# Optimization experiments

Hardware: AMD Instinct MI355X
Metric: run time of the kernel (lower is better)

Reference implementation:

```python
import jax, jax.numpy as jnp
import numpy as np

N = 50000
E = 800000
F_IN = 128
CONV_OUT = 128
CONV_LAYERS = 2
LSTM_OUT = 128
OUT_CH = 64


def setup_inputs() -> dict:
    key = jax.random.key(0)
    ks = jax.random.split(key, 16)
    s = 0.05
    inp = {
        "x": jax.random.normal(ks[0], (N, F_IN), jnp.float32),
        "edge_index": jax.random.randint(ks[1], (2, E), 0, N, dtype=jnp.int32),
        "edge_weight": jax.random.uniform(ks[2], (E,), jnp.float32),
        "H": jax.random.normal(ks[3], (1, N, LSTM_OUT), jnp.float32),
        "C": jax.random.normal(ks[4], (1, N, LSTM_OUT), jnp.float32),
        # GatedGraphConv params
        "ggc_weight": jax.random.normal(ks[5], (CONV_LAYERS, CONV_OUT, CONV_OUT), jnp.float32) * s,
        "gru_wih": jax.random.normal(ks[6], (3 * CONV_OUT, CONV_OUT), jnp.float32) * s,
        "gru_whh": jax.random.normal(ks[7], (3 * CONV_OUT, CONV_OUT), jnp.float32) * s,
        "gru_bih": jax.random.normal(ks[8], (3 * CONV_OUT,), jnp.float32) * s,
        "gru_bhh": jax.random.normal(ks[9], (3 * CONV_OUT,), jnp.float32) * s,
        # LSTM params (single layer, gate order i,f,g,o as in torch)
        "lstm_wih": jax.random.normal(ks[10], (4 * LSTM_OUT, CONV_OUT), jnp.float32) * s,
        "lstm_whh": jax.random.normal(ks[11], (4 * LSTM_OUT, LSTM_OUT), jnp.float32) * s,
        "lstm_bih": jax.random.normal(ks[12], (4 * LSTM_OUT,), jnp.float32) * s,
        "lstm_bhh": jax.random.normal(ks[13], (4 * LSTM_OUT,), jnp.float32) * s,
        # output linear
        "lin_w": jax.random.normal(ks[14], (OUT_CH, LSTM_OUT), jnp.float32) * s,
        "lin_b": jax.random.normal(ks[15], (OUT_CH,), jnp.float32) * s,
    }
    return inp


def reference(x, edge_index, edge_weight, H, C, ggc_weight, gru_wih, gru_whh,
              gru_bih, gru_bhh, lstm_wih, lstm_whh, lstm_bih, lstm_bhh, lin_w, lin_b):
    n = x.shape[0]
    out_dim = ggc_weight.shape[1]
    # GatedGraphConv: zero-pad input features up to out_dim if needed
    if x.shape[1] < out_dim:
        h = jnp.pad(x, ((0, 0), (0, out_dim - x.shape[1])))
    else:
        h = x
    src, dst = edge_index[0], edge_index[1]
    for i in range(ggc_weight.shape[0]):
        m = h @ ggc_weight[i]                      # [N, out]
        msg = m[src] * edge_weight[:, None]        # gather + weight, [E, out]
        agg = jax.ops.segment_sum(msg, dst, num_segments=n)  # scatter-add
        # GRUCell(input=agg, hidden=h)
        gi = agg @ gru_wih.T + gru_bih
        gh = h @ gru_whh.T + gru_bhh
        i_r, i_z, i_n = jnp.split(gi, 3, axis=-1)
        h_r, h_z, h_n = jnp.split(gh, 3, axis=-1)
        r = jax.nn.sigmoid(i_r + h_r)
        z = jax.nn.sigmoid(i_z + h_z)
        ncand = jnp.tanh(i_n + r * h_n)
        h = (1.0 - z) * ncand + z * h
    # single-timestep, single-layer LSTM (torch gate order i,f,g,o)
    hx, cx = H[0], C[0]
    gates = h @ lstm_wih.T + lstm_bih + hx @ lstm_whh.T + lstm_bhh
    ig, fg, gg, og = jnp.split(gates, 4, axis=-1)
    ig = jax.nn.sigmoid(ig)
    fg = jax.nn.sigmoid(fg)
    gg = jnp.tanh(gg)
    og = jax.nn.sigmoid(og)
    c_new = fg * cx + ig * gg
    h_new = og * jnp.tanh(c_new)
    out = jax.nn.relu(h_new) @ lin_w.T + lin_b     # relu then linear head
    return (out, h_new[None], c_new[None])
```

## Files before the change

### kernel.cpp

```cpp
#include <hip/hip_runtime.h>
#include <math.h>

#define N_NODES 50000
#define E_EDGES 800000
#define KD 128
#define NBLK_SCAN 196
#define RT_TILES 3125
#define CELL_RB 128
#define CELL_STRIDE (CELL_RB * 4)
#define CELL_BLOCKS 1024

typedef __attribute__((ext_vector_type(8))) short bf16x8;
typedef __attribute__((ext_vector_type(4))) float f32x4;

__device__ __forceinline__ float fsig(float x) { return 1.f / (1.f + __expf(-x)); }
__device__ __forceinline__ float ftanh(float x) { return 1.f - 2.f / (1.f + __expf(2.f * x)); }

__device__ __forceinline__ unsigned short f2bf(float f) {
    unsigned u = __float_as_uint(f);
    return (unsigned short)((u + 0x7FFFu + ((u >> 16) & 1u)) >> 16);
}
__device__ __forceinline__ float bf2f(unsigned short b) {
    return __uint_as_float(((unsigned)b) << 16);
}
__device__ __forceinline__ bf16x8 ldfrag(const unsigned short* p) {
    return *(const bf16x8*)(const void*)p;
}
__device__ __forceinline__ void stage_frag(const unsigned short* g, unsigned short* l) {
    __builtin_amdgcn_global_load_lds(
        (const __attribute__((address_space(1))) unsigned int*)g,
        (__attribute__((address_space(3))) unsigned int*)l, 16, 0, 0);
}
__device__ __forceinline__ void cell_decode(int id, int& x, int& y) {
    y = ((id >> 6) << 3) + (id & 7);
    x = (id >> 3) & 7;
}

__global__ __launch_bounds__(256) void cvt_xh(const float* __restrict__ x,
                                              const float* __restrict__ H,
                                              unsigned short* __restrict__ hb,
                                              unsigned short* __restrict__ Hxb, int n4) {
    int t = blockIdx.x * 256 + threadIdx.x;
    const float* in; unsigned short* out; int idx;
    if (t < n4) { in = x; out = hb; idx = t; }
    else if (t < 2 * n4) { in = H; out = Hxb; idx = t - n4; }
    else return;
    float4 v = ((const float4*)in)[idx];
    ushort4 o;
    o.x = f2bf(v.x); o.y = f2bf(v.y); o.z = f2bf(v.z); o.w = f2bf(v.w);
    ((ushort4*)out)[idx] = o;
}

__global__ __launch_bounds__(256) void cvt_weights(
        const float* __restrict__ b,
        const float* __restrict__ c, const float* __restrict__ d,
        const float* __restrict__ e,
        unsigned short* __restrict__ ob,
        unsigned short* __restrict__ oc, unsigned short* __restrict__ od,
        unsigned short* __restrict__ oe) {
    int t = blockIdx.x * 256 + threadIdx.x;
    const float* in; unsigned short* out; int idx;
    if      (t < 12288)  { in = b; out = ob; idx = t; }
    else if (t < 28672)  { in = c; out = oc; idx = t - 12288; }
    else if (t < 45056)  { in = d; out = od; idx = t - 28672; }
    else if (t < 47104)  { in = e; out = oe; idx = t - 45056; }
    else return;
    float4 v = ((const float4*)in)[idx];
    ushort4 o;
    o.x = f2bf(v.x); o.y = f2bf(v.y); o.z = f2bf(v.z); o.w = f2bf(v.w);
    ((ushort4*)out)[idx] = o;
}

__global__ __launch_bounds__(128) void fuse_wg_wih(const float* __restrict__ Wg,
                                                   const float* __restrict__ Wih,
                                                   unsigned short* __restrict__ WfT) {
    __shared__ float wi[128];
    const int j = blockIdx.x;
    const int l = blockIdx.y;
    const int k = threadIdx.x;
    wi[k] = Wih[j * 128 + k];
    __syncthreads();
    const float* wg = Wg + l * 16384 + k * 128;
    float s = 0.f;
#pragma unroll 8
    for (int c = 0; c < 128; c += 4) {
        float4 a = *(const float4*)(wg + c);
        s += a.x * wi[c] + a.y * wi[c + 1] + a.z * wi[c + 2] + a.w * wi[c + 3];
    }
    WfT[((size_t)l * 384 + j) * 128 + k] = f2bf(s);
}

__global__ __launch_bounds__(256) void count_deg(const int* __restrict__ ei,
                                                 int* __restrict__ deg) {
    int e = blockIdx.x * 256 + threadIdx.x;
    if (e >= E_EDGES) return;
    atomicAdd(&deg[ei[E_EDGES + e]], 1);
}

__global__ __launch_bounds__(256) void scan_p1(const int* __restrict__ deg,
                                               int* __restrict__ excl,
                                               int* __restrict__ bsum) {
    __shared__ int part[256];
    const int t = threadIdx.x;
    const int i = blockIdx.x * 256 + t;
    int v = (i < N_NODES) ? deg[i] : 0;
    part[t] = v;
    __syncthreads();
#pragma unroll
    for (int off = 1; off < 256; off <<= 1) {
        int u = (t >= off) ? part[t - off] : 0;
        __syncthreads();
        part[t] += u;
        __syncthreads();
    }
    if (i < N_NODES) excl[i] = part[t] - v;
    if (t == 255) bsum[blockIdx.x] = part[255];
}

__global__ __launch_bounds__(256) void scan_p2(int* __restrict__ bsum,
                                               int* __restrict__ rowptrN) {
    __shared__ int part[256];
    const int t = threadIdx.x;
    int v = (t < NBLK_SCAN) ? bsum[t] : 0;
    part[t] = v;
    __syncthreads();
#pragma unroll
    for (int off = 1; off < 256; off <<= 1) {
        int u = (t >= off) ? part[t - off] : 0;
        __syncthreads();
        part[t] += u;
        __syncthreads();
    }
    if (t < NBLK_SCAN) bsum[t] = part[t] - v;
    if (t == 255) *rowptrN = part[255];
}

__global__ __launch_bounds__(256) void scan_p3(const int* __restrict__ bsum,
                                               int* __restrict__ rowptr,
                                               int* __restrict__ cursor) {
    int i = blockIdx.x * 256 + threadIdx.x;
    if (i >= N_NODES) return;
    int r = rowptr[i] + bsum[blockIdx.x];
    rowptr[i] = r;
    cursor[i] = r;
}

__global__ __launch_bounds__(256) void fill_csr(const int* __restrict__ ei,
                                                const float* __restrict__ ew,
                                                int* __restrict__ cursor,
                                                int2* __restrict__ sEdge) {
    int e = blockIdx.x * 256 + threadIdx.x;
    if (e >= E_EDGES) return;
    int dst = ei[E_EDGES + e];
    int pos = atomicAdd(&cursor[dst], 1);
    int2 pk;
    pk.x = ei[e];
    pk.y = __float_as_int(ew[e]);
    sEdge[pos] = pk;
}

__global__ __launch_bounds__(256) void gather_agg_bf16(const unsigned short* __restrict__ m,
                                                       const int* __restrict__ rowptr,
                                                       const int2* __restrict__ sEdge,
                                                       unsigned short* __restrict__ agg) {
    int wid = (blockIdx.x * 256 + threadIdx.x) >> 6;
    if (wid >= N_NODES) return;
    int lane = threadIdx.x & 63;
    int q = lane >> 4, li = lane & 15;
    int f0 = li << 3;
    int e0 = rowptr[wid], e1 = rowptr[wid + 1];
    float acc[8] = {0.f, 0.f, 0.f, 0.f, 0.f, 0.f, 0.f, 0.f};
    int e = e0 + q;
    bf16x8 v = {0, 0, 0, 0, 0, 0, 0, 0};
    float w0 = 0.f;
    if (e < e1) {
        int2 pk0 = sEdge[e];
        w0 = __int_as_float(pk0.y);
        v = ldfrag(m + (size_t)pk0.x * KD + f0);
    }
    int2 pk1 = make_int2(0, 0);
    if (e + 4 < e1) pk1 = sEdge[e + 4];
    for (; e < e1; e += 4) {
        float wc = w0;
        bf16x8 vc = v;
        if (e + 4 < e1) {
            w0 = __int_as_float(pk1.y);
            v = ldfrag(m + (size_t)pk1.x * KD + f0);
        }
        if (e + 8 < e1) pk1 = sEdge[e + 8];
#pragma unroll
        for (int j = 0; j < 8; ++j)
            acc[j] += wc * bf2f((unsigned short)vc[j]);
    }
#pragma unroll
    for (int j = 0; j < 8; ++j) {
        acc[j] += __shfl_xor(acc[j], 16, 64);
        acc[j] += __shfl_xor(acc[j], 32, 64);
    }
    if (q == 0) {
        bf16x8 o;
#pragma unroll
        for (int j = 0; j < 8; ++j) o[j] = (short)f2bf(acc[j]);
        *(bf16x8*)(agg + (size_t)wid * KD + f0) = o;
    }
}

__global__ __launch_bounds__(256) void gru_fused(const unsigned short* __restrict__ Agg,
                                                 const unsigned short* __restrict__ Hin,
                                                 unsigned short* __restrict__ Hout,
                                                 const unsigned short* __restrict__ Wih,
                                                 const unsigned short* __restrict__ Whh,
                                                 const float* __restrict__ bih,
                                                 const float* __restrict__ bhh) {
    int cg, rb;
    cell_decode(blockIdx.x, cg, rb);
    __shared__ unsigned short lds[24 * 512];
    const int lane = threadIdx.x & 63, wave = threadIdx.x >> 6;
    const int rl = lane & 15, kg = lane >> 4;
    const int col0 = cg * 16;
    for (int q = wave; q < 24; q += 4) {
        int s = q >> 2, kk = q & 3;
        const unsigned short* src = (s < 3 ? Wih + (size_t)s * 128 * KD
                                           : Whh + (size_t)(s - 3) * 128 * KD)
                                    + (size_t)(col0 + rl) * KD + kk * 32 + kg * 8;
        stage_frag(src, lds + q * 512);
    }
    __syncthreads();
    const int col = col0 + rl;
    const float b_ir = bih[col], b_iz = bih[128 + col], b_in = bih[256 + col];
    const float b_hr = bhh[col], b_hz = bhh[128 + col], b_hn = bhh[256 + col];
    int rt = rb * 4 + wave;
    if (rt >= RT_TILES) return;
    bf16x8 a1[4], a2[4];
    unsigned short hvc[4];
#pragma unroll
    for (int kk = 0; kk < 4; ++kk) {
        a1[kk] = ldfrag(Agg + ((size_t)rt * 16 + rl) * KD + kk * 32 + kg * 8);
        a2[kk] = ldfrag(Hin + ((size_t)rt * 16 + rl) * KD + kk * 32 + kg * 8);
    }
#pragma unroll
    for (int p = 0; p < 4; ++p)
        hvc[p] = Hin[(size_t)(rt * 16 + kg * 4 + p) * KD + col];
    while (rt < RT_TILES) {
        const int rtn = rt + CELL_STRIDE;
        bf16x8 n1[4], n2[4];
        unsigned short hvn[4];
        if (rtn < RT_TILES) {
#pragma unroll
            for (int kk = 0; kk < 4; ++kk) {
                n1[kk] = ldfrag(Agg + ((size_t)rtn * 16 + rl) * KD + kk * 32 + kg * 8);
                n2[kk] = ldfrag(Hin + ((size_t)rtn * 16 + rl) * KD + kk * 32 + kg * 8);
            }
#pragma unroll
            for (int p = 0; p < 4; ++p)
                hvn[p] = Hin[(size_t)(rtn * 16 + kg * 4 + p) * KD + col];
        }
        f32x4 ir = {0.f,0.f,0.f,0.f}, iz = ir, in_ = ir, hr = ir, hz = ir, hn = ir;
#pragma unroll
        for (int kk = 0; kk < 4; ++kk) {
            ir  = __builtin_amdgcn_mfma_f32_16x16x32_bf16(a1[kk], ldfrag(lds + (0*4+kk)*512 + lane*8), ir,  0, 0, 0);
            iz  = __builtin_amdgcn_mfma_f32_16x16x32_bf16(a1[kk], ldfrag(lds + (1*4+kk)*512 + lane*8), iz,  0, 0, 0);
            in_ = __builtin_amdgcn_mfma_f32_16x16x32_bf16(a1[kk], ldfrag(lds + (2*4+kk)*512 + lane*8), in_, 0, 0, 0);
            hr  = __builtin_amdgcn_mfma_f32_16x16x32_bf16(a2[kk], ldfrag(lds + (3*4+kk)*512 + lane*8), hr,  0, 0, 0);
            hz  = __builtin_amdgcn_mfma_f32_16x16x32_bf16(a2[kk], ldfrag(lds + (4*4+kk)*512 + lane*8), hz,  0, 0, 0);
            hn  = __builtin_amdgcn_mfma_f32_16x16x32_bf16(a2[kk], ldfrag(lds + (5*4+kk)*512 + lane*8), hn,  0, 0, 0);
        }
#pragma unroll
        for (int p = 0; p < 4; ++p) {
            int row = rt * 16 + kg * 4 + p;
            float r = fsig(ir[p] + b_ir + hr[p] + b_hr);
            float z = fsig(iz[p] + b_iz + hz[p] + b_hz);
            float nc = ftanh(in_[p] + b_in + r * (hn[p] + b_hn));
            float hv = bf2f(hvc[p]);
            Hout[(size_t)row * KD + col] = f2bf((1.f - z) * nc + z * hv);
        }
        rt = rtn;
#pragma unroll
        for (int kk = 0; kk < 4; ++kk) { a1[kk] = n1[kk]; a2[kk] = n2[kk]; }
#pragma unroll
        for (int p = 0; p < 4; ++p) hvc[p] = hvn[p];
    }
}

__global__ __launch_bounds__(256) void lstm_fused(const unsigned short* __restrict__ Hh,
                                                  const unsigned short* __restrict__ Hx,
                                                  const float* __restrict__ Cx,
                                                  const unsigned short* __restrict__ Wih,
                                                  const unsigned short* __restrict__ Whh,
                                                  const float* __restrict__ bih,
                                                  const float* __restrict__ bhh,
                                                  float* __restrict__ h_out,
                                                  float* __restrict__ c_out,
                                                  unsigned short* __restrict__ Hrelu) {
    int cg, rb;
    cell_decode(blockIdx.x, cg, rb);
    __shared__ unsigned short lds[32 * 512];
    const int lane = threadIdx.x & 63, wave = threadIdx.x >> 6;
    const int rl = lane & 15, kg = lane >> 4;
    const int col0 = cg * 16;
    for (int q = wave; q < 32; q += 4) {
        int s = q >> 2, kk = q & 3;
        const unsigned short* src = (s < 4 ? Wih + (size_t)s * 128 * KD
                                           : Whh + (size_t)(s - 4) * 128 * KD)
                                    + (size_t)(col0 + rl) * KD + kk * 32 + kg * 8;
        stage_frag(src, lds + q * 512);
    }
    __syncthreads();
    const int col = col0 + rl;
    const float b_i = bih[col] + bhh[col];
    const float b_f = bih[128 + col] + bhh[128 + col];
    const float b_g = bih[256 + col] + bhh[256 + col];
    const float b_o = bih[384 + col] + bhh[384 + col];
    int rt = rb * 4 + wave;
    if (rt >= RT_TILES) return;
    bf16x8 a1[4], a2[4];
    float cpre[4];
#pragma unroll
    for (int kk = 0; kk < 4; ++kk) {
        a1[kk] = ldfrag(Hh + ((size_t)rt * 16 + rl) * KD + kk * 32 + kg * 8);
        a2[kk] = ldfrag(Hx + ((size_t)rt * 16 + rl) * KD + kk * 32 + kg * 8);
    }
#pragma unroll
    for (int p = 0; p < 4; ++p)
        cpre[p] = Cx[(size_t)(rt * 16 + kg * 4 + p) * KD + col];
    while (rt < RT_TILES) {
        const int rtn = rt + CELL_STRIDE;
        bf16x8 n1[4], n2[4];
        float cnx[4];
        if (rtn < RT_TILES) {
#pragma unroll
            for (int kk = 0; kk < 4; ++kk) {
                n1[kk] = ldfrag(Hh + ((size_t)rtn * 16 + rl) * KD + kk * 32 + kg * 8);
                n2[kk] = ldfrag(Hx + ((size_t)rtn * 16 + rl) * KD + kk * 32 + kg * 8);
            }
#pragma unroll
            for (int p = 0; p < 4; ++p)
                cnx[p] = Cx[(size_t)(rtn * 16 + kg * 4 + p) * KD + col];
        }
        f32x4 gi = {0.f,0.f,0.f,0.f}, gf = gi, gg = gi, go = gi;
        f32x4 hi = gi, hf = gi, hg = gi, ho = gi;
#pragma unroll
        for (int kk = 0; kk < 4; ++kk) {
            gi = __builtin_amdgcn_mfma_f32_16x16x32_bf16(a1[kk], ldfrag(lds + (0*4+kk)*512 + lane*8), gi, 0, 0, 0);
            gf = __builtin_amdgcn_mfma_f32_16x16x32_bf16(a1[kk], ldfrag(lds + (1*4+kk)*512 + lane*8), gf, 0, 0, 0);
            gg = __builtin_amdgcn_mfma_f32_16x16x32_bf16(a1[kk], ldfrag(lds + (2*4+kk)*512 + lane*8), gg, 0, 0, 0);
            go = __builtin_amdgcn_mfma_f32_16x16x32_bf16(a1[kk], ldfrag(lds + (3*4+kk)*512 + lane*8), go, 0, 0, 0);
            hi = __builtin_amdgcn_mfma_f32_16x16x32_bf16(a2[kk], ldfrag(lds + (4*4+kk)*512 + lane*8), hi, 0, 0, 0);
            hf = __builtin_amdgcn_mfma_f32_16x16x32_bf16(a2[kk], ldfrag(lds + (5*4+kk)*512 + lane*8), hf, 0, 0, 0);
            hg = __builtin_amdgcn_mfma_f32_16x16x32_bf16(a2[kk], ldfrag(lds + (6*4+kk)*512 + lane*8), hg, 0, 0, 0);
            ho = __builtin_amdgcn_mfma_f32_16x16x32_bf16(a2[kk], ldfrag(lds + (7*4+kk)*512 + lane*8), ho, 0, 0, 0);
        }
#pragma unroll
        for (int p = 0; p < 4; ++p) {
            int row = rt * 16 + kg * 4 + p;
            size_t idx = (size_t)row * KD + col;
            float ig = fsig(gi[p] + hi[p] + b_i);
            float fg = fsig(gf[p] + hf[p] + b_f);
            float gv = ftanh(gg[p] + hg[p] + b_g);
            float og = fsig(go[p] + ho[p] + b_o);
            float c = fg * cpre[p] + ig * gv;
            float hn = og * ftanh(c);
            c_out[idx] = c;
            h_out[idx] = hn;
            Hrelu[idx] = f2bf(fmaxf(hn, 0.f));
        }
        rt = rtn;
#pragma unroll
        for (int kk = 0; kk < 4; ++kk) { a1[kk] = n1[kk]; a2[kk] = n2[kk]; }
#pragma unroll
        for (int p = 0; p < 4; ++p) cpre[p] = cnx[p];
    }
}

__global__ __launch_bounds__(256) void head_gemm(const unsigned short* __restrict__ Hr,
                                                 const unsigned short* __restrict__ LinW,
                                                 const float* __restrict__ lin_b,
                                                 float* __restrict__ Out) {
    __shared__ unsigned short wlds[16 * 512];
    const int lane = threadIdx.x & 63, wave = threadIdx.x >> 6;
    const int rl = lane & 15, kg = lane >> 4;
    for (int f = wave; f < 16; f += 4) {
        int jt = f >> 2, kk = f & 3;
        stage_frag(LinW + (size_t)(jt * 16 + rl) * KD + kk * 32 + kg * 8, wlds + f * 512);
    }
    __syncthreads();
    const int stride = gridDim.x << 2;
    int rt = blockIdx.x * 4 + wave;
    if (rt >= RT_TILES) return;
    bf16x8 a[4];
#pragma unroll
    for (int kk = 0; kk < 4; ++kk)
        a[kk] = ldfrag(Hr + ((size_t)rt * 16 + rl) * KD + kk * 32 + kg * 8);
    while (rt < RT_TILES) {
        const int rtn = rt + stride;
        bf16x8 an[4];
        if (rtn < RT_TILES) {
#pragma unroll
            for (int kk = 0; kk < 4; ++kk)
                an[kk] = ldfrag(Hr + ((size_t)rtn * 16 + rl) * KD + kk * 32 + kg * 8);
        }
#pragma unroll
        for (int jt = 0; jt < 4; ++jt) {
            f32x4 acc = {0.f, 0.f, 0.f, 0.f};
#pragma unroll
            for (int kk = 0; kk < 4; ++kk)
                acc = __builtin_amdgcn_mfma_f32_16x16x32_bf16(
                    a[kk], ldfrag(wlds + (jt * 4 + kk) * 512 + lane * 8), acc, 0, 0, 0);
            int col = jt * 16 + rl;
            float b = lin_b[col];
#pragma unroll
            for (int p = 0; p < 4; ++p)
                Out[(size_t)(rt * 16 + kg * 4 + p) * 64 + col] = acc[p] + b;
        }
        rt = rtn;
#pragma unroll
        for (int kk = 0; kk < 4; ++kk) a[kk] = an[kk];
    }
}

extern "C" void kernel_launch(void* const* d_in, const int* in_sizes, int n_in,
                              void* d_out, int out_size, void* d_ws, size_t ws_size,
                              hipStream_t stream) {
    const float* x        = (const float*)d_in[0];
    const int*   ei       = (const int*)d_in[1];
    const float* ew       = (const float*)d_in[2];
    const float* H        = (const float*)d_in[3];
    const float* C        = (const float*)d_in[4];
    const float* ggc_w    = (const float*)d_in[5];
    const float* gru_wih  = (const float*)d_in[6];
    const float* gru_whh  = (const float*)d_in[7];
    const float* gru_bih  = (const float*)d_in[8];
    const float* gru_bhh  = (const float*)d_in[9];
    const float* lstm_wih = (const float*)d_in[10];
    const float* lstm_whh = (const float*)d_in[11];
    const float* lstm_bih = (const float*)d_in[12];
    const float* lstm_bhh = (const float*)d_in[13];
    const float* lin_w    = (const float*)d_in[14];
    const float* lin_b    = (const float*)d_in[15];

    float* out_head = (float*)d_out;
    float* h_out = out_head + (size_t)N_NODES * 64;
    float* c_out = h_out + (size_t)N_NODES * KD;

    char* w = (char*)d_ws;
    unsigned short* hb    = (unsigned short*)w; w += (size_t)N_NODES * KD * 2;
    unsigned short* hb1   = (unsigned short*)w; w += (size_t)N_NODES * KD * 2;
    unsigned short* Hxb   = (unsigned short*)w; w += (size_t)N_NODES * KD * 2;
    unsigned short* mb    = (unsigned short*)w; w += (size_t)N_NODES * KD * 2;
    unsigned short* aggb  = (unsigned short*)w; w += (size_t)N_NODES * KD * 2;
    unsigned short* WfT   = (unsigned short*)w; w += 2 * 384 * KD * 2;
    unsigned short* whhb  = (unsigned short*)w; w += 384 * KD * 2;
    unsigned short* lwihb = (unsigned short*)w; w += 512 * KD * 2;
    unsigned short* lwhhb = (unsigned short*)w; w += 512 * KD * 2;
    unsigned short* linwb = (unsigned short*)w; w += 64 * KD * 2;
    int*   rowptr = (int*)w; w += 50304 * 4;
    int*   cursor = (int*)w; w += 50304 * 4;
    int*   bsum   = (int*)w; w += 256 * 4;
    int2*  sEdge  = (int2*)w; w += (size_t)E_EDGES * 8;

    dim3 blk(256);
    const int EB = (E_EDGES + 255) / 256;
    const int NF4 = N_NODES * KD / 4;

    cvt_xh<<<(2 * NF4 + 255) / 256, blk, 0, stream>>>(x, H, hb, Hxb, NF4);
    cvt_weights<<<(47104 + 255) / 256, blk, 0, stream>>>(
        gru_whh, lstm_wih, lstm_whh, lin_w,
        whhb, lwihb, lwhhb, linwb);
    fuse_wg_wih<<<dim3(384, 2), 128, 0, stream>>>(ggc_w, gru_wih, WfT);

    hipMemsetAsync(cursor, 0, N_NODES * sizeof(int), stream);
    count_deg<<<EB, blk, 0, stream>>>(ei, cursor);
    scan_p1<<<NBLK_SCAN, blk, 0, stream>>>(cursor, rowptr, bsum);
    scan_p2<<<1, blk, 0, stream>>>(bsum, rowptr + N_NODES);
    scan_p3<<<NBLK_SCAN, blk, 0, stream>>>(bsum, rowptr, cursor);
    fill_csr<<<EB, blk, 0, stream>>>(ei, ew, cursor, sEdge);

    gather_agg_bf16<<<(N_NODES * 64 + 255) / 256, blk, 0, stream>>>(
        hb, rowptr, sEdge, aggb);
    gru_fused<<<CELL_BLOCKS, blk, 0, stream>>>(aggb, hb, hb1,
                                               WfT, whhb, gru_bih, gru_bhh);
    gather_agg_bf16<<<(N_NODES * 64 + 255) / 256, blk, 0, stream>>>(
        hb1, rowptr, sEdge, aggb);
    gru_fused<<<CELL_BLOCKS, blk, 0, stream>>>(aggb, hb1, hb,
                                               WfT + (size_t)384 * KD, whhb, gru_bih, gru_bhh);

    lstm_fused<<<CELL_BLOCKS, blk, 0, stream>>>(hb, Hxb, C, lwihb, lwhhb,
                                                lstm_bih, lstm_bhh, h_out, c_out, mb);
    head_gemm<<<391, blk, 0, stream>>>(mb, linwb, lin_b, out_head);
}
```

Measured before the change: 298.2 us.

## Fuse prologue kernels and build CSR via two-pass bucketed counting sort

Merges the conversion, weight-fusion and degree-count kernels into one prologue launch, removing separate launches. Replaces the per-edge global atomic CSR fill with a two-level bucket sort. Edges are first scattered into 256-node buckets using shared-memory histograms, then placed within each bucket using LDS atomics. This aims to reduce contended global atomics and scattered writes, at the cost of an extra staging pass over the edges and more workspace.

```diff
diff --git a/kernel.cpp b/kernel.cpp
--- a/kernel.cpp
+++ b/kernel.cpp
@@ -9,6 +9,8 @@
 #define CELL_RB 128
 #define CELL_STRIDE (CELL_RB * 4)
 #define CELL_BLOCKS 1024
+#define NBUCKETS 196
+#define FB_CHUNK 3125
 
 typedef __attribute__((ext_vector_type(8))) short bf16x8;
 typedef __attribute__((ext_vector_type(4))) float f32x4;
@@ -36,65 +38,62 @@
     x = (id >> 3) & 7;
 }
 
-__global__ __launch_bounds__(256) void cvt_xh(const float* __restrict__ x,
-                                              const float* __restrict__ H,
-                                              unsigned short* __restrict__ hb,
-                                              unsigned short* __restrict__ Hxb, int n4) {
-    int t = blockIdx.x * 256 + threadIdx.x;
-    const float* in; unsigned short* out; int idx;
-    if (t < n4) { in = x; out = hb; idx = t; }
-    else if (t < 2 * n4) { in = H; out = Hxb; idx = t - n4; }
-    else return;
-    float4 v = ((const float4*)in)[idx];
-    ushort4 o;
-    o.x = f2bf(v.x); o.y = f2bf(v.y); o.z = f2bf(v.z); o.w = f2bf(v.w);
-    ((ushort4*)out)[idx] = o;
-}
-
-__global__ __launch_bounds__(256) void cvt_weights(
-        const float* __restrict__ b,
-        const float* __restrict__ c, const float* __restrict__ d,
-        const float* __restrict__ e,
-        unsigned short* __restrict__ ob,
-        unsigned short* __restrict__ oc, unsigned short* __restrict__ od,
-        unsigned short* __restrict__ oe) {
-    int t = blockIdx.x * 256 + threadIdx.x;
-    const float* in; unsigned short* out; int idx;
-    if      (t < 12288)  { in = b; out = ob; idx = t; }
-    else if (t < 28672)  { in = c; out = oc; idx = t - 12288; }
-    else if (t < 45056)  { in = d; out = od; idx = t - 28672; }
-    else if (t < 47104)  { in = e; out = oe; idx = t - 45056; }
-    else return;
-    float4 v = ((const float4*)in)[idx];
-    ushort4 o;
-    o.x = f2bf(v.x); o.y = f2bf(v.y); o.z = f2bf(v.z); o.w = f2bf(v.w);
-    ((ushort4*)out)[idx] = o;
-}
-
-__global__ __launch_bounds__(128) void fuse_wg_wih(const float* __restrict__ Wg,
-                                                   const float* __restrict__ Wih,
-                                                   unsigned short* __restrict__ WfT) {
-    __shared__ float wi[128];
-    const int j = blockIdx.x;
-    const int l = blockIdx.y;
-    const int k = threadIdx.x;
-    wi[k] = Wih[j * 128 + k];
-    __syncthreads();
-    const float* wg = Wg + l * 16384 + k * 128;
-    float s = 0.f;
+#define PB_XH 12500
+#define PB_W  12684
+#define PB_F  13068
+#define PB_CD 16193
+__global__ __launch_bounds__(256) void prologue(
+        const float* __restrict__ x, const float* __restrict__ H,
+        const float* __restrict__ gru_whh, const float* __restrict__ lstm_wih,
+        const float* __restrict__ lstm_whh, const float* __restrict__ lin_w,
+        const float* __restrict__ ggc_w, const float* __restrict__ gru_wih,
+        const int* __restrict__ ei,
+        unsigned short* __restrict__ hb, unsigned short* __restrict__ Hxb,
+        unsigned short* __restrict__ whhb, unsigned short* __restrict__ lwihb,
+        unsigned short* __restrict__ lwhhb, unsigned short* __restrict__ linwb,
+        unsigned short* __restrict__ WfT, int* __restrict__ deg) {
+    const int b = blockIdx.x;
+    if (b < PB_XH) {
+        int t = b * 256 + threadIdx.x;
+        const int n4 = N_NODES * KD / 4;
+        const float* in; unsigned short* out; int idx;
+        if (t < n4) { in = x; out = hb; idx = t; }
+        else { in = H; out = Hxb; idx = t - n4; }
+        float4 v = ((const float4*)in)[idx];
+        ushort4 o;
+        o.x = f2bf(v.x); o.y = f2bf(v.y); o.z = f2bf(v.z); o.w = f2bf(v.w);
+        ((ushort4*)out)[idx] = o;
+    } else if (b < PB_W) {
+        int t = (b - PB_XH) * 256 + threadIdx.x;
+        const float* in; unsigned short* out; int idx;
+        if      (t < 12288)  { in = gru_whh;  out = whhb;  idx = t; }
+        else if (t < 28672)  { in = lstm_wih; out = lwihb; idx = t - 12288; }
+        else if (t < 45056)  { in = lstm_whh; out = lwhhb; idx = t - 28672; }
+        else if (t < 47104)  { in = lin_w;    out = linwb; idx = t - 45056; }
+        else return;
+        float4 v = ((const float4*)in)[idx];
+        ushort4 o;
+        o.x = f2bf(v.x); o.y = f2bf(v.y); o.z = f2bf(v.z); o.w = f2bf(v.w);
+        ((ushort4*)out)[idx] = o;
+    } else if (b < PB_F) {
+        int j = b - PB_W;
+        __shared__ float wi[128];
+        int k = threadIdx.x & 127;
+        int l = threadIdx.x >> 7;
+        if (threadIdx.x < 128) wi[k] = gru_wih[j * 128 + k];
+        __syncthreads();
+        const float* wg = ggc_w + l * 16384 + k * 128;
+        float s = 0.f;
 #pragma unroll 8
-    for (int c = 0; c < 128; c += 4) {
-        float4 a = *(const float4*)(wg + c);
-        s += a.x * wi[c] + a.y * wi[c + 1] + a.z * wi[c + 2] + a.w * wi[c + 3];
-    }
-    WfT[((size_t)l * 384 + j) * 128 + k] = f2bf(s);
-}
-
-__global__ __launch_bounds__(256) void count_deg(const int* __restrict__ ei,
-                                                 int* __restrict__ deg) {
-    int e = blockIdx.x * 256 + threadIdx.x;
-    if (e >= E_EDGES) return;
-    atomicAdd(&deg[ei[E_EDGES + e]], 1);
+        for (int c = 0; c < 128; c += 4) {
+            float4 a = *(const float4*)(wg + c);
+            s += a.x * wi[c] + a.y * wi[c + 1] + a.z * wi[c + 2] + a.w * wi[c + 3];
+        }
+        WfT[((size_t)l * 384 + j) * 128 + k] = f2bf(s);
+    } else {
+        int e = (b - PB_F) * 256 + threadIdx.x;
+        if (e < E_EDGES) atomicAdd(&deg[ei[E_EDGES + e]], 1);
+    }
 }
 
 __global__ __launch_bounds__(256) void scan_p1(const int* __restrict__ deg,
@@ -137,26 +136,67 @@
 
 __global__ __launch_bounds__(256) void scan_p3(const int* __restrict__ bsum,
                                                int* __restrict__ rowptr,
-                                               int* __restrict__ cursor) {
+                                               int* __restrict__ bucketCur) {
     int i = blockIdx.x * 256 + threadIdx.x;
     if (i >= N_NODES) return;
     int r = rowptr[i] + bsum[blockIdx.x];
     rowptr[i] = r;
-    cursor[i] = r;
-}
-
-__global__ __launch_bounds__(256) void fill_csr(const int* __restrict__ ei,
-                                                const float* __restrict__ ew,
-                                                int* __restrict__ cursor,
-                                                int2* __restrict__ sEdge) {
-    int e = blockIdx.x * 256 + threadIdx.x;
-    if (e >= E_EDGES) return;
-    int dst = ei[E_EDGES + e];
-    int pos = atomicAdd(&cursor[dst], 1);
-    int2 pk;
-    pk.x = ei[e];
-    pk.y = __float_as_int(ew[e]);
-    sEdge[pos] = pk;
+    if ((i & 255) == 0) bucketCur[i >> 8] = r;
+}
+
+__global__ __launch_bounds__(256) void fill_bucket(const int* __restrict__ ei,
+                                                   const float* __restrict__ ew,
+                                                   int* __restrict__ bucketCur,
+                                                   int2* __restrict__ stage_sw,
+                                                   int* __restrict__ stage_dst) {
+    __shared__ int hist[NBUCKETS];
+    __shared__ int base[NBUCKETS];
+    __shared__ int loff[NBUCKETS];
+    const int t = threadIdx.x;
+    const int e0 = blockIdx.x * FB_CHUNK;
+    const int e1 = min(e0 + FB_CHUNK, E_EDGES);
+    for (int i = t; i < NBUCKETS; i += 256) { hist[i] = 0; loff[i] = 0; }
+    __syncthreads();
+    for (int e = e0 + t; e < e1; e += 256)
+        atomicAdd(&hist[ei[E_EDGES + e] >> 8], 1);
+    __syncthreads();
+    for (int i = t; i < NBUCKETS; i += 256)
+        base[i] = hist[i] ? atomicAdd(&bucketCur[i], hist[i]) : 0;
+    __syncthreads();
+    for (int e = e0 + t; e < e1; e += 256) {
+        int dst = ei[E_EDGES + e];
+        int bk = dst >> 8;
+        int pos = base[bk] + atomicAdd(&loff[bk], 1);
+        int2 pk;
+        pk.x = ei[e];
+        pk.y = __float_as_int(ew[e]);
+        stage_sw[pos] = pk;
+        stage_dst[pos] = dst;
+    }
+}
+
+__global__ __launch_bounds__(256) void fill_final(const int* __restrict__ rowptr,
+                                                  const int2* __restrict__ stage_sw,
+                                                  const int* __restrict__ stage_dst,
+                                                  int2* __restrict__ sEdge) {
+    __shared__ int rbase[256];
+    __shared__ int cnt[256];
+    __shared__ int e1s;
+    const int b = blockIdx.x;
+    const int t = threadIdx.x;
+    const int node0 = b << 8;
+    const int nn = min(256, N_NODES - node0);
+    if (t < nn) rbase[t] = rowptr[node0 + t];
+    cnt[t] = 0;
+    if (t == 0) e1s = rowptr[min(node0 + 256, N_NODES)];
+    __syncthreads();
+    const int e0 = rbase[0];
+    const int e1 = e1s;
+    for (int e = e0 + t; e < e1; e += 256) {
+        int dl = stage_dst[e] & 255;
+        int pos = rbase[dl] + atomicAdd(&cnt[dl], 1);
+        sEdge[pos] = stage_sw[e];
+    }
 }
 
 __global__ __launch_bounds__(256) void gather_agg_bf16(const unsigned short* __restrict__ m,
@@ -453,27 +493,25 @@
     unsigned short* lwihb = (unsigned short*)w; w += 512 * KD * 2;
     unsigned short* lwhhb = (unsigned short*)w; w += 512 * KD * 2;
     unsigned short* linwb = (unsigned short*)w; w += 64 * KD * 2;
-    int*   rowptr = (int*)w; w += 50304 * 4;
-    int*   cursor = (int*)w; w += 50304 * 4;
-    int*   bsum   = (int*)w; w += 256 * 4;
-    int2*  sEdge  = (int2*)w; w += (size_t)E_EDGES * 8;
+    int*   rowptr    = (int*)w; w += 50304 * 4;
+    int*   deg       = (int*)w; w += 50304 * 4;
+    int*   bsum      = (int*)w; w += 256 * 4;
+    int*   bucketCur = (int*)w; w += 256 * 4;
+    int2*  sEdge     = (int2*)w; w += (size_t)E_EDGES * 8;
+    int2*  stage_sw  = (int2*)w; w += (size_t)E_EDGES * 8;
+    int*   stage_dst = (int*)w; w += (size_t)E_EDGES * 4;
 
     dim3 blk(256);
-    const int EB = (E_EDGES + 255) / 256;
-    const int NF4 = N_NODES * KD / 4;
-
-    cvt_xh<<<(2 * NF4 + 255) / 256, blk, 0, stream>>>(x, H, hb, Hxb, NF4);
-    cvt_weights<<<(47104 + 255) / 256, blk, 0, stream>>>(
-        gru_whh, lstm_wih, lstm_whh, lin_w,
-        whhb, lwihb, lwhhb, linwb);
-    fuse_wg_wih<<<dim3(384, 2), 128, 0, stream>>>(ggc_w, gru_wih, WfT);
-
-    hipMemsetAsync(cursor, 0, N_NODES * sizeof(int), stream);
-    count_deg<<<EB, blk, 0, stream>>>(ei, cursor);
-    scan_p1<<<NBLK_SCAN, blk, 0, stream>>>(cursor, rowptr, bsum);
+
+    hipMemsetAsync(deg, 0, N_NODES * sizeof(int), stream);
+    prologue<<<PB_CD, blk, 0, stream>>>(x, H, gru_whh, lstm_wih, lstm_whh, lin_w,
+                                        ggc_w, gru_wih, ei,
+                                        hb, Hxb, whhb, lwihb, lwhhb, linwb, WfT, deg);
+    scan_p1<<<NBLK_SCAN, blk, 0, stream>>>(deg, rowptr, bsum);
     scan_p2<<<1, blk, 0, stream>>>(bsum, rowptr + N_NODES);
-    scan_p3<<<NBLK_SCAN, blk, 0, stream>>>(bsum, rowptr, cursor);
-    fill_csr<<<EB, blk, 0, stream>>>(ei, ew, cursor, sEdge);
+    scan_p3<<<NBLK_SCAN, blk, 0, stream>>>(bsum, rowptr, bucketCur);
+    fill_bucket<<<256, blk, 0, stream>>>(ei, ew, bucketCur, stage_sw, stage_dst);
+    fill_final<<<NBUCKETS, blk, 0, stream>>>(rowptr, stage_sw, stage_dst, sEdge);
 
     gather_agg_bf16<<<(N_NODES * 64 + 255) / 256, blk, 0, stream>>>(
         hb, rowptr, sEdge, aggb);
```

Result: faster. 270.6 us (-9.2%).
